# Optimization experiments

Measured on AMD Instinct MI355X. Metric: run time of the kernel, lower is better.

Reference implementation:

```python
import jax, jax.numpy as jnp
import numpy as np

N_NODES = 50000
N_EDGES = 800000
N_GRAPHS = 256
IN_DIM, HID = 300, 256
C1, C2, C3 = 16, 64, 256


def setup_inputs() -> dict:
    key = jax.random.key(0)
    ks = jax.random.split(key, 16)
    inp = {
        "x": jax.random.normal(ks[0], (N_NODES, IN_DIM), dtype=jnp.float32),
        "edge_index": jax.random.randint(ks[1], (2, N_EDGES), 0, N_NODES, dtype=jnp.int64),
        "batch": jnp.sort(jax.random.randint(ks[2], (N_NODES,), 0, N_GRAPHS, dtype=jnp.int64)),
    }
    def lin(k, fan_in, fan_out):
        s = 1.0 / np.sqrt(fan_in)
        kw, kb = jax.random.split(k)
        return (jax.random.uniform(kw, (fan_in, fan_out), minval=-s, maxval=s, dtype=jnp.float32),
                jax.random.uniform(kb, (fan_out,), minval=-s, maxval=s, dtype=jnp.float32))
    inp["W1"], inp["b1"] = lin(ks[3], IN_DIM, HID)
    inp["W2"], inp["b2"] = lin(ks[4], HID, HID)
    inp["W3"], inp["b3"] = lin(ks[5], HID, HID)
    inp["Wc1"], inp["bc1"] = lin(ks[6], HID, C1)
    inp["Wc2"], inp["bc2"] = lin(ks[7], HID + C1, C2)
    inp["Wc3"], inp["bc3"] = lin(ks[8], HID + C2, C3)
    return inp


def reference(x, edge_index, batch, W1, b1, W2, b2, W3, b3, Wc1, bc1, Wc2, bc2, Wc3, bc3):
    N = x.shape[0]
    loop = jnp.arange(N, dtype=edge_index.dtype)
    src = jnp.concatenate([edge_index[0], loop])   # source nodes (+ self-loops)
    dst = jnp.concatenate([edge_index[1], loop])   # target nodes (+ self-loops)
    # symmetric GCN normalization: deg^{-1/2}[src] * deg^{-1/2}[dst], deg incl self-loops
    deg = jax.ops.segment_sum(jnp.ones(src.shape, x.dtype), dst, num_segments=N)
    dinv = jnp.where(deg > 0, jax.lax.rsqrt(deg), 0.0)
    norm = dinv[src] * dinv[dst]                   # [E+N]

    def gcn_conv(h, W, b):
        h = h @ W                                  # transform first (PyG order)
        msg = h[src] * norm[:, None]               # gather + scale
        return jax.ops.segment_sum(msg, dst, num_segments=N) + b  # scatter-add

    h = jax.nn.relu(gcn_conv(x, W1, b1))           # dropout = identity (eval)
    h = jax.nn.relu(gcn_conv(h, W2, b2))
    h = gcn_conv(h, W3, b3)

    # global mean pool over graphs
    cnt = jax.ops.segment_sum(jnp.ones((N,), x.dtype), batch, num_segments=N_GRAPHS)
    pooled = jax.ops.segment_sum(h, batch, num_segments=N_GRAPHS) / jnp.maximum(cnt, 1.0)[:, None]

    l1 = pooled @ Wc1 + bc1
    p1 = jax.nn.softmax(l1, axis=1)
    l2 = jnp.concatenate([pooled, p1], axis=1) @ Wc2 + bc2
    p2 = jax.nn.softmax(l2, axis=1)
    l3 = jnp.concatenate([pooled, p2], axis=1) @ Wc3 + bc3
    return (l1, l2, l3)
```

## Files before the change

kernel.cpp:

```cpp
#include <hip/hip_runtime.h>
#include <hip/hip_bf16.h>

#define N_NODES 50000
#define N_EDGES 800000
#define N_GRAPHS 256
#define IN_DIM 300
#define HID 256
#define ROWS_PAD 50048

typedef __bf16 bf16x8 __attribute__((ext_vector_type(8)));
typedef short  s16x8  __attribute__((ext_vector_type(8)));
typedef short  s16x4  __attribute__((ext_vector_type(4)));
typedef float  f32x4  __attribute__((ext_vector_type(4)));
typedef float  f32x2  __attribute__((ext_vector_type(2)));

static __device__ __forceinline__ ushort f2bf(float f) {
    union { float f; uint u; } v; v.f = f;
    uint u = v.u;
    uint r = (u + 0x7fffu + ((u >> 16) & 1u)) >> 16;
    return (ushort)r;
}
static __device__ __forceinline__ float bf2f(ushort b) {
    union { uint u; float f; } v; v.u = ((uint)b) << 16;
    return v.f;
}
static __device__ __forceinline__ unsigned char f2fp8(float f) {
    int pk = __builtin_amdgcn_cvt_pk_fp8_f32(f, f, 0, 0);
    return (unsigned char)(pk & 0xff);
}


__global__ void count_deg(const int* __restrict__ dst, int* __restrict__ cnt, int E) {
    int e = blockIdx.x * 256 + threadIdx.x;
    if (e < E) atomicAdd(&cnt[dst[e]], 1);
}

__global__ void scan1(const int* __restrict__ cnt, int* __restrict__ rp,
                      int* __restrict__ bsums, float* __restrict__ dinv, int n) {
    __shared__ int s[256];
    int i = blockIdx.x * 256 + threadIdx.x;
    int v = (i < n) ? cnt[i] : 0;
    if (i < n) dinv[i] = rsqrtf((float)(v + 1));
    s[threadIdx.x] = v;
    __syncthreads();
    for (int off = 1; off < 256; off <<= 1) {
        int t = (threadIdx.x >= off) ? s[threadIdx.x - off] : 0;
        __syncthreads();
        s[threadIdx.x] += t;
        __syncthreads();
    }
    if (i < n) rp[i] = s[threadIdx.x] - v;
    if (threadIdx.x == 255) bsums[blockIdx.x] = s[255];
}

__global__ void scan2(int* __restrict__ bsums, int nb) {
    __shared__ int s[256];
    int v = (threadIdx.x < nb) ? bsums[threadIdx.x] : 0;
    s[threadIdx.x] = v;
    __syncthreads();
    for (int off = 1; off < 256; off <<= 1) {
        int t = (threadIdx.x >= off) ? s[threadIdx.x - off] : 0;
        __syncthreads();
        s[threadIdx.x] += t;
        __syncthreads();
    }
    if (threadIdx.x < nb) bsums[threadIdx.x] = s[threadIdx.x] - v;
}

__global__ void scan3(int* __restrict__ rp, int* __restrict__ cursor,
                      const int* __restrict__ bsums, int n) {
    int i = blockIdx.x * 256 + threadIdx.x;
    if (i < n) {
        int v = rp[i] + bsums[blockIdx.x];
        rp[i] = v;
        cursor[i] = v;
    }
}

__global__ void fill_csr(const int* __restrict__ src, const int* __restrict__ dst,
                         int* __restrict__ cursor, int* __restrict__ col, int E) {
    int e = blockIdx.x * 256 + threadIdx.x;
    if (e < E) {
        int d = dst[e];
        int p = atomicAdd(&cursor[d], 1);
        col[p] = src[e];
    }
}


__global__ __launch_bounds__(256) void transpose_w3(const float* __restrict__ W1,
                                                    const float* __restrict__ W2,
                                                    const float* __restrict__ W3,
                                                    ushort* __restrict__ Wt1,
                                                    ushort* __restrict__ Wt2,
                                                    ushort* __restrict__ Wt3) {
    int b = blockIdx.x;
    int n = threadIdx.x;
    if (b < 320) {
        int k = b;
        Wt1[(size_t)n * 320 + k] = (k < IN_DIM) ? f2bf(W1[(size_t)k * 256 + n]) : (ushort)0;
    } else if (b < 576) {
        int k = b - 320;
        Wt2[(size_t)n * 256 + k] = f2bf(W2[(size_t)k * 256 + n]);
    } else {
        int k = b - 576;
        Wt3[(size_t)n * 256 + k] = f2bf(W3[(size_t)k * 256 + n]);
    }
}


template <int KP, int KACT, bool AF32>
__global__ __launch_bounds__(256, 2) void gemm_v2(const void* __restrict__ Ap,
                                                  const ushort* __restrict__ Bt,
                                                  unsigned char* __restrict__ C, int M) {
    __shared__ __align__(16) ushort As[8 * 128 * 8];
    __shared__ __align__(16) ushort Bs[8 * 256 * 8];

    int t = threadIdx.x;
    int wave = t >> 6, lane = t & 63, quad = lane >> 4, l16 = lane & 15;
    int r0 = blockIdx.x * 128;
    int arow = t & 127;
    int ahalf = t >> 7;

    f32x4 acc[8][4] = {};

    for (int kc = 0; kc < KP; kc += 64) {
#pragma unroll
        for (int i = 0; i < 8; ++i) {
            *(s16x8*)(Bs + i * 2048 + t * 8) =
                *(const s16x8*)(Bt + (size_t)t * KP + kc + i * 8);
        }
#pragma unroll
        for (int i = 0; i < 4; ++i) {
            int ks = 2 * i + ahalf;
            int kg = kc + ks * 8;
            if constexpr (AF32) {
                const float* Af = (const float*)Ap;
                int rg = r0 + arow; if (rg >= M) rg = M - 1;
                ushort tmp[8];
                if (kg + 8 <= KACT) {
                    f32x4 f0 = *(const f32x4*)(Af + (size_t)rg * KACT + kg);
                    f32x4 f1 = *(const f32x4*)(Af + (size_t)rg * KACT + kg + 4);
#pragma unroll
                    for (int j = 0; j < 4; ++j) { tmp[j] = f2bf(f0[j]); tmp[4 + j] = f2bf(f1[j]); }
                } else if (kg < KACT) {
                    f32x4 f0 = *(const f32x4*)(Af + (size_t)rg * KACT + kg);
#pragma unroll
                    for (int j = 0; j < 4; ++j) { tmp[j] = f2bf(f0[j]); tmp[4 + j] = 0; }
                } else {
#pragma unroll
                    for (int j = 0; j < 8; ++j) tmp[j] = 0;
                }
                *(s16x8*)(As + ks * 1024 + arow * 8) = *(const s16x8*)tmp;
            } else {
                const ushort* A = (const ushort*)Ap;
                *(s16x8*)(As + ks * 1024 + arow * 8) =
                    *(const s16x8*)(A + (size_t)(r0 + arow) * KP + kg);
            }
        }
        __syncthreads();

#pragma unroll
        for (int ks = 0; ks < 2; ++ks) {
            bf16x8 b[4];
#pragma unroll
            for (int ct = 0; ct < 4; ++ct)
                b[ct] = __builtin_bit_cast(bf16x8,
                    *(const s16x8*)(Bs + (ks * 4 + quad) * 2048 + (wave * 64 + ct * 16 + l16) * 8));
#pragma unroll
            for (int rt = 0; rt < 8; ++rt) {
                bf16x8 a = __builtin_bit_cast(bf16x8,
                    *(const s16x8*)(As + (ks * 4 + quad) * 1024 + (rt * 16 + l16) * 8));
#pragma unroll
                for (int ct = 0; ct < 4; ++ct)
                    acc[rt][ct] = __builtin_amdgcn_mfma_f32_16x16x32_bf16(a, b[ct], acc[rt][ct], 0, 0, 0);
            }
        }
        __syncthreads();
    }

#pragma unroll
    for (int rt = 0; rt < 8; ++rt) {
        int rowb = r0 + rt * 16 + quad * 4;
#pragma unroll
        for (int ct = 0; ct < 4; ++ct) {
            int col = wave * 64 + ct * 16 + l16;
#pragma unroll
            for (int i = 0; i < 4; ++i)
                C[(size_t)(rowb + i) * 256 + col] = f2fp8(acc[rt][ct][i]);
        }
    }
}


__global__ __launch_bounds__(256) void aggregate_fp8(const unsigned char* __restrict__ z,
                                                     ushort* __restrict__ out,
                                                     const int* __restrict__ rp,
                                                     const int* __restrict__ cnt,
                                                     const int* __restrict__ col,
                                                     const float* __restrict__ dinv,
                                                     const float* __restrict__ bias, int relu) {
    const uint* zu = (const uint*)z;
    int t = threadIdx.x;
    int wave = __builtin_amdgcn_readfirstlane(t >> 6);
    int lane = t & 63;
    int n = blockIdx.x * 4 + wave;
    int start = rp[n];
    int c = cnt[n];
    float dv = dinv[n];

    float a0 = 0.f, a1 = 0.f, a2 = 0.f, a3 = 0.f;

    int j = 0;
    for (; j + 4 <= c; j += 4) {
        int r0 = col[start + j], r1 = col[start + j + 1];
        int r2 = col[start + j + 2], r3 = col[start + j + 3];
        float w0 = dinv[r0], w1 = dinv[r1], w2 = dinv[r2], w3 = dinv[r3];
        uint v0 = zu[(size_t)r0 * 64 + lane];
        uint v1 = zu[(size_t)r1 * 64 + lane];
        uint v2 = zu[(size_t)r2 * 64 + lane];
        uint v3 = zu[(size_t)r3 * 64 + lane];
        f32x2 p, q;
        p = __builtin_amdgcn_cvt_pk_f32_fp8(v0, 0); q = __builtin_amdgcn_cvt_pk_f32_fp8(v0, 1);
        a0 += w0 * p[0]; a1 += w0 * p[1]; a2 += w0 * q[0]; a3 += w0 * q[1];
        p = __builtin_amdgcn_cvt_pk_f32_fp8(v1, 0); q = __builtin_amdgcn_cvt_pk_f32_fp8(v1, 1);
        a0 += w1 * p[0]; a1 += w1 * p[1]; a2 += w1 * q[0]; a3 += w1 * q[1];
        p = __builtin_amdgcn_cvt_pk_f32_fp8(v2, 0); q = __builtin_amdgcn_cvt_pk_f32_fp8(v2, 1);
        a0 += w2 * p[0]; a1 += w2 * p[1]; a2 += w2 * q[0]; a3 += w2 * q[1];
        p = __builtin_amdgcn_cvt_pk_f32_fp8(v3, 0); q = __builtin_amdgcn_cvt_pk_f32_fp8(v3, 1);
        a0 += w3 * p[0]; a1 += w3 * p[1]; a2 += w3 * q[0]; a3 += w3 * q[1];
    }
    for (; j < c; ++j) {
        int r = col[start + j];
        float w = dinv[r];
        uint v = zu[(size_t)r * 64 + lane];
        f32x2 p = __builtin_amdgcn_cvt_pk_f32_fp8(v, 0);
        f32x2 q = __builtin_amdgcn_cvt_pk_f32_fp8(v, 1);
        a0 += w * p[0]; a1 += w * p[1]; a2 += w * q[0]; a3 += w * q[1];
    }

    uint vs = zu[(size_t)n * 64 + lane];
    f32x2 sp = __builtin_amdgcn_cvt_pk_f32_fp8(vs, 0);
    f32x2 sq = __builtin_amdgcn_cvt_pk_f32_fp8(vs, 1);
    float sv[4] = {sp[0], sp[1], sq[0], sq[1]};
    f32x4 bv = *(const f32x4*)(bias + lane * 4);
    ushort o[4];
#pragma unroll
    for (int i = 0; i < 4; ++i) {
        float acc = (i == 0 ? a0 : i == 1 ? a1 : i == 2 ? a2 : a3);
        float r = dv * (acc + dv * sv[i]) + bv[i];
        if (relu) r = fmaxf(r, 0.f);
        o[i] = f2bf(r);
    }
    *(s16x4*)(out + (size_t)n * HID + (size_t)lane * 4) = *(const s16x4*)o;
}


__global__ __launch_bounds__(256) void pool_sum(const ushort* __restrict__ h,
                                                const int* __restrict__ batch,
                                                float* __restrict__ psum, int n) {
    int f = threadIdx.x;
    int r0 = blockIdx.x * 64;
    int rend = min(r0 + 64, n);
    if (r0 >= n) return;
    int g = batch[r0];
    float acc = 0.f;
    for (int r = r0; r < rend; ++r) {
        int gr = batch[r];
        if (gr != g) {
            atomicAdd(&psum[g * HID + f], acc);
            acc = 0.f;
            g = gr;
        }
        acc += bf2f(h[(size_t)r * HID + f]);
    }
    atomicAdd(&psum[g * HID + f], acc);
}


__global__ __launch_bounds__(256) void head_k(const float* __restrict__ psum,
                                              const int* __restrict__ batch, int n,
                                              const float* __restrict__ Wc1, const float* __restrict__ bc1,
                                              const float* __restrict__ Wc2, const float* __restrict__ bc2,
                                              const float* __restrict__ Wc3, const float* __restrict__ bc3,
                                              float* __restrict__ out) {
    int g = blockIdx.x;
    int t = threadIdx.x;
    __shared__ float pr[256];
    __shared__ float l1s[16], p1s[16];
    __shared__ float l2s[64], p2s[64];
    int lo = 0, hi = n;
    while (lo < hi) { int mid = (lo + hi) >> 1; if (batch[mid] < g) lo = mid + 1; else hi = mid; }
    int start = lo;
    lo = start; hi = n;
    while (lo < hi) { int mid = (lo + hi) >> 1; if (batch[mid] < g + 1) lo = mid + 1; else hi = mid; }
    int c = lo - start;
    float inv_c = 1.f / (float)max(c, 1);
    pr[t] = psum[g * 256 + t] * inv_c;
    __syncthreads();
    if (t < 16) {
        float a = bc1[t];
        for (int k = 0; k < 256; ++k) a += pr[k] * Wc1[k * 16 + t];
        l1s[t] = a;
        out[g * 16 + t] = a;
    }
    __syncthreads();
    if (t == 0) {
        float m = -1e30f;
        for (int j = 0; j < 16; ++j) m = fmaxf(m, l1s[j]);
        float s = 0.f;
        for (int j = 0; j < 16; ++j) { float e = expf(l1s[j] - m); p1s[j] = e; s += e; }
        float inv = 1.f / s;
        for (int j = 0; j < 16; ++j) p1s[j] *= inv;
    }
    __syncthreads();
    if (t < 64) {
        float a = bc2[t];
        for (int k = 0; k < 256; ++k) a += pr[k] * Wc2[k * 64 + t];
        for (int k = 0; k < 16; ++k) a += p1s[k] * Wc2[(256 + k) * 64 + t];
        l2s[t] = a;
        out[4096 + g * 64 + t] = a;
    }
    __syncthreads();
    if (t == 0) {
        float m = -1e30f;
        for (int j = 0; j < 64; ++j) m = fmaxf(m, l2s[j]);
        float s = 0.f;
        for (int j = 0; j < 64; ++j) { float e = expf(l2s[j] - m); p2s[j] = e; s += e; }
        float inv = 1.f / s;
        for (int j = 0; j < 64; ++j) p2s[j] *= inv;
    }
    __syncthreads();
    {
        float a = bc3[t];
        for (int k = 0; k < 256; ++k) a += pr[k] * Wc3[k * 256 + t];
        for (int k = 0; k < 64; ++k) a += p2s[k] * Wc3[(256 + k) * 256 + t];
        out[4096 + 16384 + g * 256 + t] = a;
    }
}


extern "C" void kernel_launch(void* const* d_in, const int* in_sizes, int n_in,
                              void* d_out, int out_size, void* d_ws, size_t ws_size,
                              hipStream_t stream) {
    const float* x    = (const float*)d_in[0];
    const int*   ei   = (const int*)d_in[1];
    const int*   batch= (const int*)d_in[2];
    const float* W1 = (const float*)d_in[3];  const float* b1 = (const float*)d_in[4];
    const float* W2 = (const float*)d_in[5];  const float* b2 = (const float*)d_in[6];
    const float* W3 = (const float*)d_in[7];  const float* b3 = (const float*)d_in[8];
    const float* Wc1= (const float*)d_in[9];  const float* bc1= (const float*)d_in[10];
    const float* Wc2= (const float*)d_in[11]; const float* bc2= (const float*)d_in[12];
    const float* Wc3= (const float*)d_in[13]; const float* bc3= (const float*)d_in[14];
    float* out = (float*)d_out;

    const int N = N_NODES, E = N_EDGES, G = N_GRAPHS;

    char* ws = (char*)d_ws;
    size_t off = 0;
    auto alloc = [&](size_t bytes) -> void* {
        void* p = ws + off;
        off = (off + bytes + 255) & ~(size_t)255;
        return p;
    };
    unsigned char* z = (unsigned char*)alloc((size_t)ROWS_PAD * HID);
    ushort* hb   = (ushort*)alloc((size_t)ROWS_PAD * HID * 2);
    ushort* Wt1  = (ushort*)alloc((size_t)256 * 320 * 2);
    ushort* Wt2  = (ushort*)alloc((size_t)256 * 256 * 2);
    ushort* Wt3  = (ushort*)alloc((size_t)256 * 256 * 2);
    int*   cnt    = (int*)alloc((size_t)N * 4);
    int*   rp     = (int*)alloc((size_t)N * 4);
    int*   cursor = (int*)alloc((size_t)N * 4);
    float* dinv   = (float*)alloc((size_t)N * 4);
    int*   col    = (int*)alloc((size_t)E * 4);
    float* psum   = (float*)alloc((size_t)G * HID * 4);
    int*   bsums  = (int*)alloc(256 * 4);
    (void)ws_size;

    const int* src = ei;
    const int* dst = ei + E;

    hipMemsetAsync(cnt, 0, (size_t)N * 4, stream);
    hipMemsetAsync(psum, 0, (size_t)G * HID * 4, stream);
    count_deg<<<(E + 255) / 256, 256, 0, stream>>>(dst, cnt, E);
    const int NB = (N + 255) / 256;
    scan1<<<NB, 256, 0, stream>>>(cnt, rp, bsums, dinv, N);
    scan2<<<1, 256, 0, stream>>>(bsums, NB);
    scan3<<<NB, 256, 0, stream>>>(rp, cursor, bsums, N);
    fill_csr<<<(E + 255) / 256, 256, 0, stream>>>(src, dst, cursor, col, E);

    transpose_w3<<<832, 256, 0, stream>>>(W1, W2, W3, Wt1, Wt2, Wt3);

    const int GB = ROWS_PAD / 128;
    gemm_v2<320, IN_DIM, true><<<GB, 256, 0, stream>>>(x, Wt1, z, N);
    aggregate_fp8<<<N / 4, 256, 0, stream>>>(z, hb, rp, cnt, col, dinv, b1, 1);
    gemm_v2<256, 256, false><<<GB, 256, 0, stream>>>(hb, Wt2, z, N);
    aggregate_fp8<<<N / 4, 256, 0, stream>>>(z, hb, rp, cnt, col, dinv, b2, 1);
    gemm_v2<256, 256, false><<<GB, 256, 0, stream>>>(hb, Wt3, z, N);
    aggregate_fp8<<<N / 4, 256, 0, stream>>>(z, hb, rp, cnt, col, dinv, b3, 0);

    pool_sum<<<ROWS_PAD / 64, 256, 0, stream>>>(hb, batch, psum, N);
    head_k<<<G, 256, 0, stream>>>(psum, batch, N, Wc1, bc1, Wc2, bc2, Wc3, bc3, out);
}
```

Measured before the change: 453.0 us.

## Merge preprocessing kernels and overlap CSR fill with first GEMM

```diff
diff --git a/kernel.cpp b/kernel.cpp
--- a/kernel.cpp
+++ b/kernel.cpp
@@ -7,6 +7,8 @@
 #define IN_DIM 300
 #define HID 256
 #define ROWS_PAD 50048
+#define GEMM_GB 391
+#define FILL_NB 3125
 
 typedef __bf16 bf16x8 __attribute__((ext_vector_type(8)));
 typedef short  s16x8  __attribute__((ext_vector_type(8)));
@@ -30,70 +32,14 @@
 }
 
 
-__global__ void count_deg(const int* __restrict__ dst, int* __restrict__ cnt, int E) {
-    int e = blockIdx.x * 256 + threadIdx.x;
-    if (e < E) atomicAdd(&cnt[dst[e]], 1);
-}
-
-__global__ void scan1(const int* __restrict__ cnt, int* __restrict__ rp,
-                      int* __restrict__ bsums, float* __restrict__ dinv, int n) {
-    __shared__ int s[256];
-    int i = blockIdx.x * 256 + threadIdx.x;
-    int v = (i < n) ? cnt[i] : 0;
-    if (i < n) dinv[i] = rsqrtf((float)(v + 1));
-    s[threadIdx.x] = v;
-    __syncthreads();
-    for (int off = 1; off < 256; off <<= 1) {
-        int t = (threadIdx.x >= off) ? s[threadIdx.x - off] : 0;
-        __syncthreads();
-        s[threadIdx.x] += t;
-        __syncthreads();
-    }
-    if (i < n) rp[i] = s[threadIdx.x] - v;
-    if (threadIdx.x == 255) bsums[blockIdx.x] = s[255];
-}
-
-__global__ void scan2(int* __restrict__ bsums, int nb) {
-    __shared__ int s[256];
-    int v = (threadIdx.x < nb) ? bsums[threadIdx.x] : 0;
-    s[threadIdx.x] = v;
-    __syncthreads();
-    for (int off = 1; off < 256; off <<= 1) {
-        int t = (threadIdx.x >= off) ? s[threadIdx.x - off] : 0;
-        __syncthreads();
-        s[threadIdx.x] += t;
-        __syncthreads();
-    }
-    if (threadIdx.x < nb) bsums[threadIdx.x] = s[threadIdx.x] - v;
-}
-
-__global__ void scan3(int* __restrict__ rp, int* __restrict__ cursor,
-                      const int* __restrict__ bsums, int n) {
-    int i = blockIdx.x * 256 + threadIdx.x;
-    if (i < n) {
-        int v = rp[i] + bsums[blockIdx.x];
-        rp[i] = v;
-        cursor[i] = v;
-    }
-}
-
-__global__ void fill_csr(const int* __restrict__ src, const int* __restrict__ dst,
-                         int* __restrict__ cursor, int* __restrict__ col, int E) {
-    int e = blockIdx.x * 256 + threadIdx.x;
-    if (e < E) {
-        int d = dst[e];
-        int p = atomicAdd(&cursor[d], 1);
-        col[p] = src[e];
-    }
-}
-
-
-__global__ __launch_bounds__(256) void transpose_w3(const float* __restrict__ W1,
-                                                    const float* __restrict__ W2,
-                                                    const float* __restrict__ W3,
-                                                    ushort* __restrict__ Wt1,
-                                                    ushort* __restrict__ Wt2,
-                                                    ushort* __restrict__ Wt3) {
+__global__ __launch_bounds__(256) void pre_k(const float* __restrict__ W1,
+                                             const float* __restrict__ W2,
+                                             const float* __restrict__ W3,
+                                             ushort* __restrict__ Wt1,
+                                             ushort* __restrict__ Wt2,
+                                             ushort* __restrict__ Wt3,
+                                             const int* __restrict__ dst,
+                                             int* __restrict__ cnt) {
     int b = blockIdx.x;
     int n = threadIdx.x;
     if (b < 320) {
@@ -102,23 +48,67 @@
     } else if (b < 576) {
         int k = b - 320;
         Wt2[(size_t)n * 256 + k] = f2bf(W2[(size_t)k * 256 + n]);
-    } else {
+    } else if (b < 832) {
         int k = b - 576;
         Wt3[(size_t)n * 256 + k] = f2bf(W3[(size_t)k * 256 + n]);
+    } else {
+        int e = (b - 832) * 256 + n;
+        if (e < N_EDGES) atomicAdd(&cnt[dst[e]], 1);
+    }
+}
+
+
+__global__ void scan1(const int* __restrict__ cnt, int* __restrict__ rp,
+                      int* __restrict__ bsums, float* __restrict__ dinv, int n) {
+    __shared__ int s[256];
+    int i = blockIdx.x * 256 + threadIdx.x;
+    int v = (i < n) ? cnt[i] : 0;
+    if (i < n) dinv[i] = rsqrtf((float)(v + 1));
+    s[threadIdx.x] = v;
+    __syncthreads();
+    for (int off = 1; off < 256; off <<= 1) {
+        int t = (threadIdx.x >= off) ? s[threadIdx.x - off] : 0;
+        __syncthreads();
+        s[threadIdx.x] += t;
+        __syncthreads();
+    }
+    if (i < n) rp[i] = s[threadIdx.x] - v;
+    if (threadIdx.x == 255) bsums[blockIdx.x] = s[255];
+}
+
+__global__ void scan2(int* __restrict__ bsums, int nb) {
+    __shared__ int s[256];
+    int v = (threadIdx.x < nb) ? bsums[threadIdx.x] : 0;
+    s[threadIdx.x] = v;
+    __syncthreads();
+    for (int off = 1; off < 256; off <<= 1) {
+        int t = (threadIdx.x >= off) ? s[threadIdx.x - off] : 0;
+        __syncthreads();
+        s[threadIdx.x] += t;
+        __syncthreads();
+    }
+    if (threadIdx.x < nb) bsums[threadIdx.x] = s[threadIdx.x] - v;
+}
+
+__global__ void scan3(int* __restrict__ rp, int* __restrict__ cursor,
+                      const int* __restrict__ bsums, int n) {
+    int i = blockIdx.x * 256 + threadIdx.x;
+    if (i < n) {
+        int v = rp[i] + bsums[blockIdx.x];
+        rp[i] = v;
+        cursor[i] = v;
     }
 }
 
 
 template <int KP, int KACT, bool AF32>
-__global__ __launch_bounds__(256, 2) void gemm_v2(const void* __restrict__ Ap,
-                                                  const ushort* __restrict__ Bt,
-                                                  unsigned char* __restrict__ C, int M) {
-    __shared__ __align__(16) ushort As[8 * 128 * 8];
-    __shared__ __align__(16) ushort Bs[8 * 256 * 8];
-
+static __device__ __forceinline__ void gemm_body(int bx, const void* __restrict__ Ap,
+                                                 const ushort* __restrict__ Bt,
+                                                 unsigned char* __restrict__ C, int M,
+                                                 ushort* As, ushort* Bs) {
     int t = threadIdx.x;
     int wave = t >> 6, lane = t & 63, quad = lane >> 4, l16 = lane & 15;
-    int r0 = blockIdx.x * 128;
+    int r0 = bx * 128;
     int arow = t & 127;
     int ahalf = t >> 7;
 
@@ -188,6 +178,37 @@
 #pragma unroll
             for (int i = 0; i < 4; ++i)
                 C[(size_t)(rowb + i) * 256 + col] = f2fp8(acc[rt][ct][i]);
+        }
+    }
+}
+
+template <int KP, int KACT, bool AF32>
+__global__ __launch_bounds__(256, 2) void gemm_k(const void* __restrict__ Ap,
+                                                 const ushort* __restrict__ Bt,
+                                                 unsigned char* __restrict__ C, int M) {
+    __shared__ __align__(16) ushort As[8 * 128 * 8];
+    __shared__ __align__(16) ushort Bs[8 * 256 * 8];
+    gemm_body<KP, KACT, AF32>(blockIdx.x, Ap, Bt, C, M, As, Bs);
+}
+
+__global__ __launch_bounds__(256, 2) void gemm1_fill(const float* __restrict__ x,
+                                                     const ushort* __restrict__ Wt1,
+                                                     unsigned char* __restrict__ C, int M,
+                                                     const int* __restrict__ src,
+                                                     const int* __restrict__ dst,
+                                                     int* __restrict__ cursor,
+                                                     int* __restrict__ col) {
+    __shared__ __align__(16) ushort As[8 * 128 * 8];
+    __shared__ __align__(16) ushort Bs[8 * 256 * 8];
+    int b = blockIdx.x;
+    if (b < GEMM_GB) {
+        gemm_body<320, IN_DIM, true>(b, x, Wt1, C, M, As, Bs);
+    } else {
+        int e = (b - GEMM_GB) * 256 + threadIdx.x;
+        if (e < N_EDGES) {
+            int d = dst[e];
+            int p = atomicAdd(&cursor[d], 1);
+            col[p] = src[e];
         }
     }
 }
@@ -382,21 +403,20 @@
 
     hipMemsetAsync(cnt, 0, (size_t)N * 4, stream);
     hipMemsetAsync(psum, 0, (size_t)G * HID * 4, stream);
-    count_deg<<<(E + 255) / 256, 256, 0, stream>>>(dst, cnt, E);
+
+    pre_k<<<832 + FILL_NB, 256, 0, stream>>>(W1, W2, W3, Wt1, Wt2, Wt3, dst, cnt);
+
     const int NB = (N + 255) / 256;
     scan1<<<NB, 256, 0, stream>>>(cnt, rp, bsums, dinv, N);
     scan2<<<1, 256, 0, stream>>>(bsums, NB);
     scan3<<<NB, 256, 0, stream>>>(rp, cursor, bsums, N);
-    fill_csr<<<(E + 255) / 256, 256, 0, stream>>>(src, dst, cursor, col, E);
-
-    transpose_w3<<<832, 256, 0, stream>>>(W1, W2, W3, Wt1, Wt2, Wt3);
-
-    const int GB = ROWS_PAD / 128;
-    gemm_v2<320, IN_DIM, true><<<GB, 256, 0, stream>>>(x, Wt1, z, N);
+
+    gemm1_fill<<<GEMM_GB + FILL_NB, 256, 0, stream>>>(x, Wt1, z, N, src, dst, cursor, col);
+
     aggregate_fp8<<<N / 4, 256, 0, stream>>>(z, hb, rp, cnt, col, dinv, b1, 1);
-    gemm_v2<256, 256, false><<<GB, 256, 0, stream>>>(hb, Wt2, z, N);
+    gemm_k<256, 256, false><<<GEMM_GB, 256, 0, stream>>>(hb, Wt2, z, N);
     aggregate_fp8<<<N / 4, 256, 0, stream>>>(z, hb, rp, cnt, col, dinv, b2, 1);
-    gemm_v2<256, 256, false><<<GB, 256, 0, stream>>>(hb, Wt3, z, N);
+    gemm_k<256, 256, false><<<GEMM_GB, 256, 0, stream>>>(hb, Wt3, z, N);
     aggregate_fp8<<<N / 4, 256, 0, stream>>>(z, hb, rp, cnt, col, dinv, b3, 0);
 
     pool_sum<<<ROWS_PAD / 64, 256, 0, stream>>>(hb, batch, psum, N);
```

New measurement: 425.6 us. -6.1%, faster.
